# Kernel tuning notes

Measured on AMD Instinct MI355X. Metric: run time of the kernel, lower is better.

Reference implementation:

```python
import jax, jax.numpy as jnp
import numpy as np

B, D, C, S = 65536, 128, 10, 2
LAMBDA_E, LAMBDA_OD = 0.1, 0.036
GAMMA_E, GAMMA_OD = 2.0, 2.0
STEP_SIZE = 1000.0


def setup_inputs() -> dict:
    key = jax.random.key(0)
    ks = jax.random.split(key, 12)
    inp = {
        "mean_t": jax.random.normal(ks[0], (B, D), jnp.float32),
        "mean_s": jax.random.normal(ks[1], (B, D), jnp.float32),
        "log_std_t": jax.random.normal(ks[2], (B, D), jnp.float32),
        "log_std_s": jax.random.normal(ks[3], (B, D), jnp.float32),
        "y_zt": jax.random.normal(ks[4], (B, C), jnp.float32),
        "s_zt": jax.random.normal(ks[5], (B, S), jnp.float32),
        "eps_prior_t": jax.random.normal(ks[6], (B, D), jnp.float32),
        "eps_prior_s": jax.random.normal(ks[7], (B, D), jnp.float32),
        "eps_t": jax.random.normal(ks[8], (B, D), jnp.float32),
        "eps_s": jax.random.normal(ks[9], (B, D), jnp.float32),
        "target": jax.random.randint(ks[10], (B,), 0, C, jnp.int64),
        "current_step": 500,
    }
    return inp


def _kld_batchmean(log_p, t):
    # torch KLDivLoss(reduction='batchmean'): sum(t * (log t - log_p)) / batch
    return jnp.sum(t * (jnp.log(t) - log_p)) / t.shape[0]


def reference(mean_t, mean_s, log_std_t, log_std_s, y_zt, s_zt,
              eps_prior_t, eps_prior_s, eps_t, eps_s, target, current_step):
    # CIFAR10 branch: cross entropy on task logits
    logp_y = jax.nn.log_softmax(y_zt, axis=1)
    L_t = -jnp.mean(jnp.take_along_axis(logp_y, target[:, None], axis=1))

    # entropy loss on sensitive discriminator output
    sm = jax.nn.softmax(s_zt, axis=1)
    lsm = jax.nn.log_softmax(s_zt, axis=1)
    Loss_e = -jnp.sum(sm * lsm) / s_zt.shape[0]

    # prior samples: N(0, I) and N(1, I)  (mean_tensors(zeros, ones))
    prior_t = eps_prior_t            # mean 0
    prior_s = 1.0 + eps_prior_s      # mean 1

    # encoder samples: MVN(mean, diag(exp(log_std))) -> std = exp(0.5*log_std)
    # torch .sample() is non-differentiable -> stop_gradient
    enc_t = jax.lax.stop_gradient(mean_t + jnp.exp(0.5 * log_std_t) * eps_t)
    enc_s = jax.lax.stop_gradient(mean_s + jnp.exp(0.5 * log_std_s) * eps_s)

    L_zt = _kld_batchmean(jax.nn.log_softmax(prior_t, axis=1), jax.nn.softmax(enc_t, axis=1))
    L_zs = _kld_batchmean(jax.nn.log_softmax(prior_s, axis=1), jax.nn.softmax(enc_s, axis=1))

    frac = current_step / STEP_SIZE
    lam_e = LAMBDA_E * GAMMA_E ** frac
    lam_od = LAMBDA_OD * GAMMA_OD ** frac
    return L_t + lam_e * Loss_e + lam_od * (L_zt + L_zs)
```

## Files before the change

kernel.cpp:

```cpp
#include <hip/hip_runtime.h>
#include <math.h>

#define BATCH 65536
#define NCLS  10
#define NCE   64
#define NKL   2048
#define NBTOT (NKL + NCE)
#define KL_WAVES (NKL * 4)
#define CE_WAVES (NCE * 4)


typedef float vf4 __attribute__((ext_vector_type(4)));


__global__ __launch_bounds__(256, 4) void crit_main(
    const float* __restrict__ mean_t,      const float* __restrict__ mean_s,
    const float* __restrict__ log_std_t,   const float* __restrict__ log_std_s,
    const float* __restrict__ y_zt,        const float* __restrict__ s_zt,
    const float* __restrict__ eps_prior_t, const float* __restrict__ eps_prior_s,
    const float* __restrict__ eps_t,       const float* __restrict__ eps_s,
    const int*   __restrict__ target,
    double*      __restrict__ ws_partial)
{
    const int tid = threadIdx.x;
    const int wid = tid >> 6;
    const int lane = tid & 63;

    if (blockIdx.x >= NCE) {
        const int sub  = lane & 15;
        const int grp  = (lane >> 4) & 3;
        const int gwave = (blockIdx.x - NCE) * 4 + wid;
        const int rowbase = gwave * 8;

        const vf4* MT = (const vf4*)mean_t;
        const vf4* LT = (const vf4*)log_std_t;
        const vf4* ET = (const vf4*)eps_t;
        const vf4* PT = (const vf4*)eps_prior_t;
        const vf4* MS = (const vf4*)mean_s;
        const vf4* LS = (const vf4*)log_std_s;
        const vf4* ES = (const vf4*)eps_s;
        const vf4* PS = (const vf4*)eps_prior_s;

        int i0[2], i1[2];
        #pragma unroll
        for (int k = 0; k < 2; ++k) {
            const int row = rowbase + k * 4 + grp;
            i0[k] = row * 32 + sub;
            i1[k] = i0[k] + 16;
        }

        vf4 mt[2][2], lt[2][2], et[2][2], pt[2][2];
        vf4 ms[2][2], ls[2][2], es[2][2], ps[2][2];
        #pragma unroll
        for (int k = 0; k < 2; ++k) {
            mt[k][0] = __builtin_nontemporal_load(&MT[i0[k]]);
            mt[k][1] = __builtin_nontemporal_load(&MT[i1[k]]);
            lt[k][0] = __builtin_nontemporal_load(&LT[i0[k]]);
            lt[k][1] = __builtin_nontemporal_load(&LT[i1[k]]);
            et[k][0] = __builtin_nontemporal_load(&ET[i0[k]]);
            et[k][1] = __builtin_nontemporal_load(&ET[i1[k]]);
            pt[k][0] = __builtin_nontemporal_load(&PT[i0[k]]);
            pt[k][1] = __builtin_nontemporal_load(&PT[i1[k]]);
            ms[k][0] = __builtin_nontemporal_load(&MS[i0[k]]);
            ms[k][1] = __builtin_nontemporal_load(&MS[i1[k]]);
            ls[k][0] = __builtin_nontemporal_load(&LS[i0[k]]);
            ls[k][1] = __builtin_nontemporal_load(&LS[i1[k]]);
            es[k][0] = __builtin_nontemporal_load(&ES[i0[k]]);
            es[k][1] = __builtin_nontemporal_load(&ES[i1[k]]);
            ps[k][0] = __builtin_nontemporal_load(&PS[i0[k]]);
            ps[k][1] = __builtin_nontemporal_load(&PS[i1[k]]);
        }
        __builtin_amdgcn_sched_barrier(0);

        float red[2][6];
        #pragma unroll
        for (int k = 0; k < 2; ++k) {
            #pragma unroll
            for (int j = 0; j < 6; ++j) red[k][j] = 0.0f;
            #pragma unroll
            for (int h = 0; h < 2; ++h) {
                #pragma unroll
                for (int c = 0; c < 4; ++c) {
                    const float enc_t = fmaf(__expf(0.5f * lt[k][h][c]), et[k][h][c], mt[k][h][c]);
                    const float enc_s = fmaf(__expf(0.5f * ls[k][h][c]), es[k][h][c], ms[k][h][c]);
                    const float xt = __expf(enc_t);
                    const float xs = __expf(enc_s);
                    red[k][0] += xt;
                    red[k][1] += __expf(pt[k][h][c]);
                    red[k][2] += xt * (enc_t - pt[k][h][c]);
                    red[k][3] += xs;
                    red[k][4] += __expf(ps[k][h][c]);
                    red[k][5] += xs * (enc_s - ps[k][h][c]);
                }
            }
        }

        #pragma unroll
        for (int m = 8; m >= 1; m >>= 1) {
            #pragma unroll
            for (int k = 0; k < 2; ++k) {
                #pragma unroll
                for (int j = 0; j < 6; ++j) red[k][j] += __shfl_xor(red[k][j], m, 64);
            }
        }

        float kl = 0.0f;
        #pragma unroll
        for (int k = 0; k < 2; ++k) {
            const float rt = 1.0f / red[k][0];
            const float rs = 1.0f / red[k][3];
            kl += red[k][2] * rt + __logf(red[k][1] * rt)
                + red[k][5] * rs + __logf(red[k][4] * rs);
        }
        kl += __shfl_xor(kl, 16, 64);
        kl += __shfl_xor(kl, 32, 64);
        if (lane == 0) ws_partial[gwave] = (double)kl;
    } else {
        double ce_d = 0.0, H_d = 0.0;
        const int gtid = blockIdx.x * 256 + tid;
        #pragma unroll
        for (int k = 0; k < 4; ++k) {
            const int r = gtid + k * 16384;
            const float* yr = y_zt + (size_t)r * NCLS;
            const float2 y0 = *(const float2*)(yr + 0);
            const float2 y1 = *(const float2*)(yr + 2);
            const float2 y2 = *(const float2*)(yr + 4);
            const float2 y3 = *(const float2*)(yr + 6);
            const float2 y4 = *(const float2*)(yr + 8);
            const float2 s2 = *(const float2*)(s_zt + (size_t)r * 2);
            const int    t  = target[r];

            float yt = y0.x;
            yt = (t == 1) ? y0.y : yt;
            yt = (t == 2) ? y1.x : yt;
            yt = (t == 3) ? y1.y : yt;
            yt = (t == 4) ? y2.x : yt;
            yt = (t == 5) ? y2.y : yt;
            yt = (t == 6) ? y3.x : yt;
            yt = (t == 7) ? y3.y : yt;
            yt = (t == 8) ? y4.x : yt;
            yt = (t == 9) ? y4.y : yt;

            const float Z = (__expf(y0.x) + __expf(y0.y))
                          + (__expf(y1.x) + __expf(y1.y))
                          + (__expf(y2.x) + __expf(y2.y))
                          + (__expf(y3.x) + __expf(y3.y))
                          + (__expf(y4.x) + __expf(y4.y));
            ce_d += (double)(__logf(Z) - yt);

            const float za = __expf(s2.x), zb = __expf(s2.y);
            const float Zs = za + zb;
            const float lses = __logf(Zs);
            H_d += (double)(-((za / Zs) * (s2.x - lses) + (zb / Zs) * (s2.y - lses)));
        }

        #pragma unroll
        for (int m = 32; m >= 1; m >>= 1) {
            ce_d += __shfl_xor(ce_d, m, 64);
            H_d  += __shfl_xor(H_d,  m, 64);
        }
        if (lane == 0) {
            const int cw = blockIdx.x * 4 + wid;
            ws_partial[KL_WAVES + cw]            = ce_d;
            ws_partial[KL_WAVES + CE_WAVES + cw] = H_d;
        }
    }
}

__global__ __launch_bounds__(256) void crit_reduce(
    const double* __restrict__ ws_partial,
    const int*    __restrict__ step_ptr,
    float*        __restrict__ out)
{
    const int tid = threadIdx.x;
    double k = 0.0;
    for (int i = tid; i < KL_WAVES; i += 256) k += ws_partial[i];
    double c = ws_partial[KL_WAVES + tid];
    double h = ws_partial[KL_WAVES + CE_WAVES + tid];

    __shared__ double sc[256], sh_[256], sk[256];
    sc[tid] = c; sh_[tid] = h; sk[tid] = k;
    __syncthreads();
    for (int s = 128; s > 0; s >>= 1) {
        if (tid < s) { sc[tid] += sc[tid + s]; sh_[tid] += sh_[tid + s]; sk[tid] += sk[tid + s]; }
        __syncthreads();
    }
    if (tid == 0) {
        double frac  = (double)step_ptr[0] / 1000.0;
        double lam_e  = 0.1   * exp2(frac);
        double lam_od = 0.036 * exp2(frac);
        out[0] = (float)((sc[0] + lam_e * sh_[0] + lam_od * sk[0]) / (double)BATCH);
    }
}

extern "C" void kernel_launch(void* const* d_in, const int* in_sizes, int n_in,
                              void* d_out, int out_size, void* d_ws, size_t ws_size,
                              hipStream_t stream) {
    const float* mean_t      = (const float*)d_in[0];
    const float* mean_s      = (const float*)d_in[1];
    const float* log_std_t   = (const float*)d_in[2];
    const float* log_std_s   = (const float*)d_in[3];
    const float* y_zt        = (const float*)d_in[4];
    const float* s_zt        = (const float*)d_in[5];
    const float* eps_prior_t = (const float*)d_in[6];
    const float* eps_prior_s = (const float*)d_in[7];
    const float* eps_t       = (const float*)d_in[8];
    const float* eps_s       = (const float*)d_in[9];
    const int*   target      = (const int*)d_in[10];
    const int*   step_ptr    = (const int*)d_in[11];

    double* ws_partial = (double*)d_ws;
    float*  out        = (float*)d_out;

    crit_main<<<NBTOT, 256, 0, stream>>>(
        mean_t, mean_s, log_std_t, log_std_s, y_zt, s_zt,
        eps_prior_t, eps_prior_s, eps_t, eps_s, target, ws_partial);
    crit_reduce<<<1, 256, 0, stream>>>(ws_partial, step_ptr, out);
}
```

Baseline: 255.7 us.

## Merge CE/entropy work into KL blocks and reduce per block

```diff
diff --git a/kernel.cpp b/kernel.cpp
--- a/kernel.cpp
+++ b/kernel.cpp
@@ -3,17 +3,13 @@
 
 #define BATCH 65536
 #define NCLS  10
-#define NCE   64
-#define NKL   2048
-#define NBTOT (NKL + NCE)
-#define KL_WAVES (NKL * 4)
-#define CE_WAVES (NCE * 4)
+#define NBLK  2048
 
 
 typedef float vf4 __attribute__((ext_vector_type(4)));
 
 
-__global__ __launch_bounds__(256, 4) void crit_main(
+__global__ __launch_bounds__(256, 2) void crit_main(
     const float* __restrict__ mean_t,      const float* __restrict__ mean_s,
     const float* __restrict__ log_std_t,   const float* __restrict__ log_std_s,
     const float* __restrict__ y_zt,        const float* __restrict__ s_zt,
@@ -26,144 +22,138 @@
     const int wid = tid >> 6;
     const int lane = tid & 63;
 
-    if (blockIdx.x >= NCE) {
-        const int sub  = lane & 15;
-        const int grp  = (lane >> 4) & 3;
-        const int gwave = (blockIdx.x - NCE) * 4 + wid;
-        const int rowbase = gwave * 8;
-
-        const vf4* MT = (const vf4*)mean_t;
-        const vf4* LT = (const vf4*)log_std_t;
-        const vf4* ET = (const vf4*)eps_t;
-        const vf4* PT = (const vf4*)eps_prior_t;
-        const vf4* MS = (const vf4*)mean_s;
-        const vf4* LS = (const vf4*)log_std_s;
-        const vf4* ES = (const vf4*)eps_s;
-        const vf4* PS = (const vf4*)eps_prior_s;
-
-        int i0[2], i1[2];
+    const int sub  = lane & 15;
+    const int grp  = (lane >> 4) & 3;
+    const int gwave = blockIdx.x * 4 + wid;
+    const int rowbase = gwave * 8;
+
+    const vf4* MT = (const vf4*)mean_t;
+    const vf4* LT = (const vf4*)log_std_t;
+    const vf4* ET = (const vf4*)eps_t;
+    const vf4* PT = (const vf4*)eps_prior_t;
+    const vf4* MS = (const vf4*)mean_s;
+    const vf4* LS = (const vf4*)log_std_s;
+    const vf4* ES = (const vf4*)eps_s;
+    const vf4* PS = (const vf4*)eps_prior_s;
+
+    int i0[2], i1[2];
+    #pragma unroll
+    for (int k = 0; k < 2; ++k) {
+        const int row = rowbase + k * 4 + grp;
+        i0[k] = row * 32 + sub;
+        i1[k] = i0[k] + 16;
+    }
+
+    vf4 mt[2][2], lt[2][2], et[2][2], pt[2][2];
+    vf4 ms[2][2], ls[2][2], es[2][2], ps[2][2];
+    #pragma unroll
+    for (int k = 0; k < 2; ++k) {
+        mt[k][0] = MT[i0[k]];  mt[k][1] = MT[i1[k]];
+        lt[k][0] = LT[i0[k]];  lt[k][1] = LT[i1[k]];
+        et[k][0] = ET[i0[k]];  et[k][1] = ET[i1[k]];
+        pt[k][0] = PT[i0[k]];  pt[k][1] = PT[i1[k]];
+        ms[k][0] = MS[i0[k]];  ms[k][1] = MS[i1[k]];
+        ls[k][0] = LS[i0[k]];  ls[k][1] = LS[i1[k]];
+        es[k][0] = ES[i0[k]];  es[k][1] = ES[i1[k]];
+        ps[k][0] = PS[i0[k]];  ps[k][1] = PS[i1[k]];
+    }
+    __builtin_amdgcn_sched_barrier(0);
+
+    float red[2][6];
+    #pragma unroll
+    for (int k = 0; k < 2; ++k) {
         #pragma unroll
-        for (int k = 0; k < 2; ++k) {
-            const int row = rowbase + k * 4 + grp;
-            i0[k] = row * 32 + sub;
-            i1[k] = i0[k] + 16;
+        for (int j = 0; j < 6; ++j) red[k][j] = 0.0f;
+        #pragma unroll
+        for (int h = 0; h < 2; ++h) {
+            #pragma unroll
+            for (int c = 0; c < 4; ++c) {
+                const float enc_t = fmaf(__expf(0.5f * lt[k][h][c]), et[k][h][c], mt[k][h][c]);
+                const float enc_s = fmaf(__expf(0.5f * ls[k][h][c]), es[k][h][c], ms[k][h][c]);
+                const float xt = __expf(enc_t);
+                const float xs = __expf(enc_s);
+                red[k][0] += xt;
+                red[k][1] += __expf(pt[k][h][c]);
+                red[k][2] += xt * (enc_t - pt[k][h][c]);
+                red[k][3] += xs;
+                red[k][4] += __expf(ps[k][h][c]);
+                red[k][5] += xs * (enc_s - ps[k][h][c]);
+            }
         }
-
-        vf4 mt[2][2], lt[2][2], et[2][2], pt[2][2];
-        vf4 ms[2][2], ls[2][2], es[2][2], ps[2][2];
-        #pragma unroll
-        for (int k = 0; k < 2; ++k) {
-            mt[k][0] = __builtin_nontemporal_load(&MT[i0[k]]);
-            mt[k][1] = __builtin_nontemporal_load(&MT[i1[k]]);
-            lt[k][0] = __builtin_nontemporal_load(&LT[i0[k]]);
-            lt[k][1] = __builtin_nontemporal_load(&LT[i1[k]]);
-            et[k][0] = __builtin_nontemporal_load(&ET[i0[k]]);
-            et[k][1] = __builtin_nontemporal_load(&ET[i1[k]]);
-            pt[k][0] = __builtin_nontemporal_load(&PT[i0[k]]);
-            pt[k][1] = __builtin_nontemporal_load(&PT[i1[k]]);
-            ms[k][0] = __builtin_nontemporal_load(&MS[i0[k]]);
-            ms[k][1] = __builtin_nontemporal_load(&MS[i1[k]]);
-            ls[k][0] = __builtin_nontemporal_load(&LS[i0[k]]);
-            ls[k][1] = __builtin_nontemporal_load(&LS[i1[k]]);
-            es[k][0] = __builtin_nontemporal_load(&ES[i0[k]]);
-            es[k][1] = __builtin_nontemporal_load(&ES[i1[k]]);
-            ps[k][0] = __builtin_nontemporal_load(&PS[i0[k]]);
-            ps[k][1] = __builtin_nontemporal_load(&PS[i1[k]]);
-        }
-        __builtin_amdgcn_sched_barrier(0);
-
-        float red[2][6];
+    }
+
+    #pragma unroll
+    for (int m = 8; m >= 1; m >>= 1) {
         #pragma unroll
         for (int k = 0; k < 2; ++k) {
             #pragma unroll
-            for (int j = 0; j < 6; ++j) red[k][j] = 0.0f;
-            #pragma unroll
-            for (int h = 0; h < 2; ++h) {
-                #pragma unroll
-                for (int c = 0; c < 4; ++c) {
-                    const float enc_t = fmaf(__expf(0.5f * lt[k][h][c]), et[k][h][c], mt[k][h][c]);
-                    const float enc_s = fmaf(__expf(0.5f * ls[k][h][c]), es[k][h][c], ms[k][h][c]);
-                    const float xt = __expf(enc_t);
-                    const float xs = __expf(enc_s);
-                    red[k][0] += xt;
-                    red[k][1] += __expf(pt[k][h][c]);
-                    red[k][2] += xt * (enc_t - pt[k][h][c]);
-                    red[k][3] += xs;
-                    red[k][4] += __expf(ps[k][h][c]);
-                    red[k][5] += xs * (enc_s - ps[k][h][c]);
-                }
-            }
+            for (int j = 0; j < 6; ++j) red[k][j] += __shfl_xor(red[k][j], m, 64);
         }
-
-        #pragma unroll
-        for (int m = 8; m >= 1; m >>= 1) {
-            #pragma unroll
-            for (int k = 0; k < 2; ++k) {
-                #pragma unroll
-                for (int j = 0; j < 6; ++j) red[k][j] += __shfl_xor(red[k][j], m, 64);
-            }
-        }
-
-        float kl = 0.0f;
-        #pragma unroll
-        for (int k = 0; k < 2; ++k) {
-            const float rt = 1.0f / red[k][0];
-            const float rs = 1.0f / red[k][3];
-            kl += red[k][2] * rt + __logf(red[k][1] * rt)
-                + red[k][5] * rs + __logf(red[k][4] * rs);
-        }
-        kl += __shfl_xor(kl, 16, 64);
-        kl += __shfl_xor(kl, 32, 64);
-        if (lane == 0) ws_partial[gwave] = (double)kl;
-    } else {
-        double ce_d = 0.0, H_d = 0.0;
-        const int gtid = blockIdx.x * 256 + tid;
-        #pragma unroll
-        for (int k = 0; k < 4; ++k) {
-            const int r = gtid + k * 16384;
-            const float* yr = y_zt + (size_t)r * NCLS;
-            const float2 y0 = *(const float2*)(yr + 0);
-            const float2 y1 = *(const float2*)(yr + 2);
-            const float2 y2 = *(const float2*)(yr + 4);
-            const float2 y3 = *(const float2*)(yr + 6);
-            const float2 y4 = *(const float2*)(yr + 8);
-            const float2 s2 = *(const float2*)(s_zt + (size_t)r * 2);
-            const int    t  = target[r];
-
-            float yt = y0.x;
-            yt = (t == 1) ? y0.y : yt;
-            yt = (t == 2) ? y1.x : yt;
-            yt = (t == 3) ? y1.y : yt;
-            yt = (t == 4) ? y2.x : yt;
-            yt = (t == 5) ? y2.y : yt;
-            yt = (t == 6) ? y3.x : yt;
-            yt = (t == 7) ? y3.y : yt;
-            yt = (t == 8) ? y4.x : yt;
-            yt = (t == 9) ? y4.y : yt;
-
-            const float Z = (__expf(y0.x) + __expf(y0.y))
-                          + (__expf(y1.x) + __expf(y1.y))
-                          + (__expf(y2.x) + __expf(y2.y))
-                          + (__expf(y3.x) + __expf(y3.y))
-                          + (__expf(y4.x) + __expf(y4.y));
-            ce_d += (double)(__logf(Z) - yt);
-
-            const float za = __expf(s2.x), zb = __expf(s2.y);
-            const float Zs = za + zb;
-            const float lses = __logf(Zs);
-            H_d += (double)(-((za / Zs) * (s2.x - lses) + (zb / Zs) * (s2.y - lses)));
-        }
-
-        #pragma unroll
-        for (int m = 32; m >= 1; m >>= 1) {
-            ce_d += __shfl_xor(ce_d, m, 64);
-            H_d  += __shfl_xor(H_d,  m, 64);
-        }
-        if (lane == 0) {
-            const int cw = blockIdx.x * 4 + wid;
-            ws_partial[KL_WAVES + cw]            = ce_d;
-            ws_partial[KL_WAVES + CE_WAVES + cw] = H_d;
-        }
+    }
+
+    float kl = 0.0f;
+    #pragma unroll
+    for (int k = 0; k < 2; ++k) {
+        const float rt = 1.0f / red[k][0];
+        const float rs = 1.0f / red[k][3];
+        kl += red[k][2] * rt + __logf(red[k][1] * rt)
+            + red[k][5] * rs + __logf(red[k][4] * rs);
+    }
+    kl += __shfl_xor(kl, 16, 64);
+    kl += __shfl_xor(kl, 32, 64);
+
+    double ce_d = 0.0, H_d = 0.0;
+    if (lane < 8) {
+        const int r = blockIdx.x * 32 + wid * 8 + lane;
+        const float* yr = y_zt + (size_t)r * NCLS;
+        const float2 y0 = *(const float2*)(yr + 0);
+        const float2 y1 = *(const float2*)(yr + 2);
+        const float2 y2 = *(const float2*)(yr + 4);
+        const float2 y3 = *(const float2*)(yr + 6);
+        const float2 y4 = *(const float2*)(yr + 8);
+        const float2 s2 = *(const float2*)(s_zt + (size_t)r * 2);
+        const int    t  = target[r];
+
+        float yt = y0.x;
+        yt = (t == 1) ? y0.y : yt;
+        yt = (t == 2) ? y1.x : yt;
+        yt = (t == 3) ? y1.y : yt;
+        yt = (t == 4) ? y2.x : yt;
+        yt = (t == 5) ? y2.y : yt;
+        yt = (t == 6) ? y3.x : yt;
+        yt = (t == 7) ? y3.y : yt;
+        yt = (t == 8) ? y4.x : yt;
+        yt = (t == 9) ? y4.y : yt;
+
+        const float Z = (__expf(y0.x) + __expf(y0.y))
+                      + (__expf(y1.x) + __expf(y1.y))
+                      + (__expf(y2.x) + __expf(y2.y))
+                      + (__expf(y3.x) + __expf(y3.y))
+                      + (__expf(y4.x) + __expf(y4.y));
+        ce_d = (double)(__logf(Z) - yt);
+
+        const float za = __expf(s2.x), zb = __expf(s2.y);
+        const float Zs = za + zb;
+        const float lses = __logf(Zs);
+        H_d = (double)(-((za / Zs) * (s2.x - lses) + (zb / Zs) * (s2.y - lses)));
+    }
+    #pragma unroll
+    for (int m = 4; m >= 1; m >>= 1) {
+        ce_d += __shfl_xor(ce_d, m, 64);
+        H_d  += __shfl_xor(H_d,  m, 64);
+    }
+
+    __shared__ double sred[4][3];
+    if (lane == 0) {
+        sred[wid][0] = ce_d;
+        sred[wid][1] = H_d;
+        sred[wid][2] = (double)kl;
+    }
+    __syncthreads();
+    if (tid == 0) {
+        ws_partial[blockIdx.x * 3 + 0] = sred[0][0] + sred[1][0] + sred[2][0] + sred[3][0];
+        ws_partial[blockIdx.x * 3 + 1] = sred[0][1] + sred[1][1] + sred[2][1] + sred[3][1];
+        ws_partial[blockIdx.x * 3 + 2] = sred[0][2] + sred[1][2] + sred[2][2] + sred[3][2];
     }
 }
 
@@ -173,11 +163,12 @@
     float*        __restrict__ out)
 {
     const int tid = threadIdx.x;
-    double k = 0.0;
-    for (int i = tid; i < KL_WAVES; i += 256) k += ws_partial[i];
-    double c = ws_partial[KL_WAVES + tid];
-    double h = ws_partial[KL_WAVES + CE_WAVES + tid];
-
+    double c = 0.0, h = 0.0, k = 0.0;
+    for (int i = tid; i < NBLK; i += 256) {
+        c += ws_partial[3 * i + 0];
+        h += ws_partial[3 * i + 1];
+        k += ws_partial[3 * i + 2];
+    }
     __shared__ double sc[256], sh_[256], sk[256];
     sc[tid] = c; sh_[tid] = h; sk[tid] = k;
     __syncthreads();
@@ -212,7 +203,7 @@
     double* ws_partial = (double*)d_ws;
     float*  out        = (float*)d_out;
 
-    crit_main<<<NBTOT, 256, 0, stream>>>(
+    crit_main<<<NBLK, 256, 0, stream>>>(
         mean_t, mean_s, log_std_t, log_std_s, y_zt, s_zt,
         eps_prior_t, eps_prior_s, eps_t, eps_s, target, ws_partial);
     crit_reduce<<<1, 256, 0, stream>>>(ws_partial, step_ptr, out);
```

Measured after the change: 269.6 us. 1.05x slower.
